# Optimization experiments

Hardware: AMD Instinct MI355X
Metric: run time of the kernel (lower is better)

The kernel has to match this reference:

```python
import jax, jax.numpy as jnp
import numpy as np
from jax import lax

T, H, I, E, K = 1024, 1024, 512, 16, 4


def setup_inputs() -> dict:
    key = jax.random.key(0)
    k1, k2, k3, k4, k5 = jax.random.split(key, 5)
    hidden_states = jax.random.normal(k1, (T, H), dtype=jnp.float32)
    top_k_index = jax.random.randint(k2, (T, K), 0, E)
    top_k_weights = jax.random.uniform(k3, (T, K), dtype=jnp.float32)
    gate_up_proj = jax.random.normal(k4, (E, 2 * I, H), dtype=jnp.float32) * 0.02
    down_proj = jax.random.normal(k5, (E, H, I), dtype=jnp.float32) * 0.02
    return {
        "hidden_states": hidden_states,
        "top_k_index": top_k_index,
        "top_k_weights": top_k_weights,
        "gate_up_proj": gate_up_proj,
        "down_proj": down_proj,
    }


def reference(hidden_states, top_k_index, top_k_weights, gate_up_proj, down_proj):
    num_experts = gate_up_proj.shape[0]
    # combine[t, e] = sum_k top_k_weights[t, k] * [top_k_index[t, k] == e]
    # Expert output is linear in the routing weight, so summing weights over
    # duplicate (token, expert) hits matches the original index_add_ exactly.
    one_hot = jax.nn.one_hot(top_k_index, num_experts, dtype=hidden_states.dtype)  # [T, K, E]
    combine = jnp.einsum("tke,tk->te", one_hot, top_k_weights)  # [T, E]

    def expert_step(acc, xs):
        w_gu, w_d, c = xs  # [2I, H], [H, I], [T]
        gu = hidden_states @ w_gu.T          # [T, 2I]
        gate, up = jnp.split(gu, 2, axis=-1)
        h = jax.nn.silu(gate) * up            # [T, I]
        out = h @ w_d.T                       # [T, H]
        return acc + out * c[:, None], None

    final, _ = lax.scan(
        expert_step,
        jnp.zeros_like(hidden_states),
        (gate_up_proj, down_proj, combine.T),
    )
    return final
```

## Files before the change

### kernel.cpp

```cpp
#include <hip/hip_runtime.h>
#include <hip/hip_bf16.h>
#include <cstdint>
#include <cstddef>

#define T_TOK 1024
#define HDIM  1024
#define IDIM  512
#define NEXP  16
#define TOPK  4
#define CAP   1024

typedef __bf16 bf16;
typedef __attribute__((ext_vector_type(8))) __bf16 bf16x8;
typedef __attribute__((ext_vector_type(4))) __bf16 bf16x4;
typedef __attribute__((ext_vector_type(4))) float f32x4;

__device__ __forceinline__ void lds_load16(void* lds_dst, const void* g_src) {
  __builtin_amdgcn_global_load_lds(
      (__attribute__((address_space(1))) unsigned int*)(void*)(g_src),
      (__attribute__((address_space(3))) unsigned int*)(lds_dst),
      16, 0, 0);
}

__device__ __forceinline__ bf16x4 cvt4(float4 a) {
  bf16x4 o;
  o[0] = (bf16)a.x; o[1] = (bf16)a.y; o[2] = (bf16)a.z; o[3] = (bf16)a.w;
  return o;
}


#define CVT_BLOCKS (T_TOK * HDIM / 4 / 256)

__global__ void prep_kernel(const float* __restrict__ hid_f, bf16* __restrict__ hid_b,
                            const int* __restrict__ idx, const float* __restrict__ w,
                            int* __restrict__ etk, float* __restrict__ ew,
                            int* __restrict__ cntpad, float* __restrict__ out) {
  __shared__ int cnt;
  const int b = blockIdx.x;
  const int tid = threadIdx.x;
  if (b < CVT_BLOCKS) {
    int i = b * 256 + tid;
    float4 v = ((const float4*)hid_f)[i];
    ((bf16x4*)hid_b)[i] = cvt4(v);
    ((float4*)out)[i] = make_float4(0.f, 0.f, 0.f, 0.f);
    if (b == 0)
      ((bf16x4*)(hid_b + (size_t)T_TOK * HDIM))[tid] = cvt4(make_float4(0.f, 0.f, 0.f, 0.f));
    return;
  }
  const int e = b - CVT_BLOCKS;
  if (tid == 0) cnt = 0;
  __syncthreads();
  for (int j = tid; j < T_TOK * TOPK; j += blockDim.x) {
    if (idx[j] == e) {
      int slot = atomicAdd(&cnt, 1);
      if (slot < CAP) { etk[e * CAP + slot] = j; ew[e * CAP + slot] = w[j]; }
    }
  }
  __syncthreads();
  int c = cnt < CAP ? cnt : CAP;
  int p = (c + 127) & ~127;
  for (int j = c + tid; j < p; j += blockDim.x) {
    etk[e * CAP + j] = (T_TOK << 2);
    ew[e * CAP + j] = 0.f;
  }
  if (tid == 0) cntpad[e] = p;
}


__global__ __launch_bounds__(256, 3) void gemm1_kernel(
    const bf16* __restrict__ hid,
    const float* __restrict__ gup,
    const int* __restrict__ etk, const float* __restrict__ ew,
    const int* __restrict__ cntpad,
    bf16* __restrict__ hsc) {
  __shared__ __align__(16) bf16 As[2][128 * 64];
  __shared__ __align__(16) bf16 Bs[2][64 * 64];
  const int e = blockIdx.y, z = blockIdx.z;
  const int ntiles = cntpad[e] >> 7;
  const int n0 = blockIdx.x * 32;
  const int ebase = e * CAP;
  const int tid = threadIdx.x, lane = tid & 63, wid = tid >> 6;
  const int wm = (wid >> 1) * 64, wi = (wid & 1) * 16;
  const int lcol = lane & 15, lquad = lane >> 4;
  const int l7 = lcol & 7;
  const int srow = tid >> 3;
  const int swz = ((tid & 7) ^ (srow & 7)) * 8;
  const int r = tid >> 2;
  const int c0 = (tid & 3) * 4;
  const int grow = (r < 32) ? (n0 + r) : (IDIM + n0 + (r - 32));
  const float* gB = gup + (size_t)e * (2 * IDIM) * HDIM + (size_t)grow * HDIM + c0;
  int wb[4];
#pragma unroll
  for (int j = 0; j < 4; ++j) {
    int c = c0 + 16 * j;
    wb[j] = (((c >> 3) ^ (r & 7)) * 8) + (c & 7);
  }
  const int bst = r * 64;

  for (int mt = z; mt < ntiles; mt += 3) {
    const int mrow = ebase + mt * 128;
    const bf16* gA[4];
#pragma unroll
    for (int q = 0; q < 4; ++q)
      gA[q] = hid + (size_t)(etk[mrow + srow + 32 * q] >> 2) * HDIM + swz;
    f32x4 aG[4], aU[4];
#pragma unroll
    for (int mf = 0; mf < 4; ++mf) {
      aG[mf] = f32x4{0.f, 0.f, 0.f, 0.f};
      aU[mf] = f32x4{0.f, 0.f, 0.f, 0.f};
    }
    {
      float4 bv[4];
#pragma unroll
      for (int j = 0; j < 4; ++j) bv[j] = *(const float4*)(gB + 16 * j);
#pragma unroll
      for (int q = 0; q < 4; ++q)
        lds_load16(&As[0][tid * 8 + q * 2048], gA[q]);
#pragma unroll
      for (int j = 0; j < 4; ++j)
        *(bf16x4*)&Bs[0][bst + wb[j]] = cvt4(bv[j]);
    }
    __syncthreads();
#pragma unroll 2
    for (int k = 0; k < 16; ++k) {
      const int cur = k & 1, nxt = cur ^ 1;
      float4 bn[4];
      if (k < 15) {
#pragma unroll
        for (int q = 0; q < 4; ++q)
          lds_load16(&As[nxt][tid * 8 + q * 2048], gA[q] + (k + 1) * 64);
#pragma unroll
        for (int j = 0; j < 4; ++j)
          bn[j] = *(const float4*)(gB + (k + 1) * 64 + 16 * j);
      }
      __builtin_amdgcn_s_setprio(1);
#pragma unroll
      for (int ks = 0; ks < 2; ++ks) {
        const int lch = ks * 4 + lquad;
        const int sw = (lch ^ l7) * 8;
        bf16x8 bg = *(const bf16x8*)&Bs[cur][(wi + lcol) * 64 + sw];
        bf16x8 bu = *(const bf16x8*)&Bs[cur][(32 + wi + lcol) * 64 + sw];
#pragma unroll
        for (int mf = 0; mf < 4; ++mf) {
          bf16x8 af = *(const bf16x8*)&As[cur][(wm + mf * 16 + lcol) * 64 + sw];
          aG[mf] = __builtin_amdgcn_mfma_f32_16x16x32_bf16(af, bg, aG[mf], 0, 0, 0);
          aU[mf] = __builtin_amdgcn_mfma_f32_16x16x32_bf16(af, bu, aU[mf], 0, 0, 0);
        }
      }
      __builtin_amdgcn_s_setprio(0);
      if (k < 15) {
#pragma unroll
        for (int j = 0; j < 4; ++j)
          *(bf16x4*)&Bs[nxt][bst + wb[j]] = cvt4(bn[j]);
      }
      __syncthreads();
    }
#pragma unroll
    for (int mf = 0; mf < 4; ++mf) {
#pragma unroll
      for (int rr = 0; rr < 4; ++rr) {
        const int erow = mt * 128 + wm + mf * 16 + lquad * 4 + rr;
        const float wgt = ew[ebase + erow];
        float g = aG[mf][rr], u = aU[mf][rr];
        float s = g / (1.f + __expf(-g));
        hsc[(size_t)(ebase + erow) * IDIM + n0 + wi + lcol] = (bf16)(s * u * wgt);
      }
    }
  }
}


__global__ __launch_bounds__(256, 3) void gemm2_kernel(
    const bf16* __restrict__ hsc,
    const float* __restrict__ down,
    const int* __restrict__ etk, const int* __restrict__ cntpad,
    float* __restrict__ out) {
  __shared__ __align__(16) bf16 As[2][128 * 64];
  __shared__ __align__(16) bf16 Bs[2][64 * 64];
  const int e = blockIdx.y, z = blockIdx.z;
  const int ntiles = cntpad[e] >> 7;
  const int n0 = blockIdx.x * 64;
  const int ebase = e * CAP;
  const int tid = threadIdx.x, lane = tid & 63, wid = tid >> 6;
  const int wm = (wid >> 1) * 64, wh = (wid & 1) * 32;
  const int lcol = lane & 15, lquad = lane >> 4;
  const int l7 = lcol & 7;
  const int srow = tid >> 3;
  const int swz = ((tid & 7) ^ (srow & 7)) * 8;
  const int r = tid >> 2;
  const int c0 = (tid & 3) * 4;
  const float* gB = down + (size_t)e * HDIM * IDIM + (size_t)(n0 + r) * IDIM + c0;
  int wb[4];
#pragma unroll
  for (int j = 0; j < 4; ++j) {
    int c = c0 + 16 * j;
    wb[j] = (((c >> 3) ^ (r & 7)) * 8) + (c & 7);
  }
  const int bst = r * 64;

  for (int mt = z; mt < ntiles; mt += 3) {
    const size_t rbase = (size_t)(ebase + mt * 128);
    const bf16* gA[4];
#pragma unroll
    for (int q = 0; q < 4; ++q)
      gA[q] = hsc + (rbase + srow + 32 * q) * IDIM + swz;
    f32x4 acc[4][2];
#pragma unroll
    for (int mf = 0; mf < 4; ++mf) {
      acc[mf][0] = f32x4{0.f, 0.f, 0.f, 0.f};
      acc[mf][1] = f32x4{0.f, 0.f, 0.f, 0.f};
    }
    {
      float4 bv[4];
#pragma unroll
      for (int j = 0; j < 4; ++j) bv[j] = *(const float4*)(gB + 16 * j);
#pragma unroll
      for (int q = 0; q < 4; ++q)
        lds_load16(&As[0][tid * 8 + q * 2048], gA[q]);
#pragma unroll
      for (int j = 0; j < 4; ++j)
        *(bf16x4*)&Bs[0][bst + wb[j]] = cvt4(bv[j]);
    }
    __syncthreads();
#pragma unroll 2
    for (int k = 0; k < 8; ++k) {
      const int cur = k & 1, nxt = cur ^ 1;
      float4 bn[4];
      if (k < 7) {
#pragma unroll
        for (int q = 0; q < 4; ++q)
          lds_load16(&As[nxt][tid * 8 + q * 2048], gA[q] + (k + 1) * 64);
#pragma unroll
        for (int j = 0; j < 4; ++j)
          bn[j] = *(const float4*)(gB + (k + 1) * 64 + 16 * j);
      }
      __builtin_amdgcn_s_setprio(1);
#pragma unroll
      for (int ks = 0; ks < 2; ++ks) {
        const int lch = ks * 4 + lquad;
        const int sw = (lch ^ l7) * 8;
        bf16x8 b0 = *(const bf16x8*)&Bs[cur][(wh + lcol) * 64 + sw];
        bf16x8 b1 = *(const bf16x8*)&Bs[cur][(wh + 16 + lcol) * 64 + sw];
#pragma unroll
        for (int mf = 0; mf < 4; ++mf) {
          bf16x8 af = *(const bf16x8*)&As[cur][(wm + mf * 16 + lcol) * 64 + sw];
          acc[mf][0] = __builtin_amdgcn_mfma_f32_16x16x32_bf16(af, b0, acc[mf][0], 0, 0, 0);
          acc[mf][1] = __builtin_amdgcn_mfma_f32_16x16x32_bf16(af, b1, acc[mf][1], 0, 0, 0);
        }
      }
      __builtin_amdgcn_s_setprio(0);
      if (k < 7) {
#pragma unroll
        for (int j = 0; j < 4; ++j)
          *(bf16x4*)&Bs[nxt][bst + wb[j]] = cvt4(bn[j]);
      }
      __syncthreads();
    }
#pragma unroll
    for (int mf = 0; mf < 4; ++mf) {
#pragma unroll
      for (int rr = 0; rr < 4; ++rr) {
        const int row = mt * 128 + wm + mf * 16 + lquad * 4 + rr;
        const int tk = etk[ebase + row];
        const int tok = tk >> 2;
        if (tok < T_TOK) {
          float* orow = out + (size_t)tok * HDIM + n0 + wh + lcol;
          atomicAdd(orow, acc[mf][0][rr]);
          atomicAdd(orow + 16, acc[mf][1][rr]);
        }
      }
    }
  }
}


extern "C" void kernel_launch(void* const* d_in, const int* in_sizes, int n_in,
                              void* d_out, int out_size, void* d_ws, size_t ws_size,
                              hipStream_t stream) {
  const float* hid_f  = (const float*)d_in[0];
  const int*   idx    = (const int*)d_in[1];
  const float* tw     = (const float*)d_in[2];
  const float* gup_f  = (const float*)d_in[3];
  const float* down_f = (const float*)d_in[4];
  float* out = (float*)d_out;

  uint8_t* ws = (uint8_t*)d_ws;
  size_t off = 0;
  bf16* hid_b = (bf16*)(ws + off);   off += (size_t)(T_TOK + 1) * HDIM * 2;
  int*  etk   = (int*)(ws + off);    off += (size_t)NEXP * CAP * 4;
  float* ewt  = (float*)(ws + off);  off += (size_t)NEXP * CAP * 4;
  int* cntpad = (int*)(ws + off);    off += 256;
  bf16* hsc   = (bf16*)(ws + off);

  prep_kernel<<<dim3(CVT_BLOCKS + NEXP), dim3(256), 0, stream>>>(
      hid_f, hid_b, idx, tw, etk, ewt, cntpad, out);
  gemm1_kernel<<<dim3(IDIM / 32, NEXP, 3), dim3(256), 0, stream>>>(
      hid_b, gup_f, etk, ewt, cntpad, hsc);
  gemm2_kernel<<<dim3(HDIM / 64, NEXP, 3), dim3(256), 0, stream>>>(
      hsc, down_f, etk, cntpad, out);
}
```

Baseline: 176.9 us.

## Flatten expert tiles into grid and stream B operand through registers

Both GEMM kernels now launch one block per (expert, 128-row tile) through a flattened lookup over the padded per-expert counts. This replaces the old grid-stride loop over a fixed z dimension, which left blocks idle for experts with few tiles. The weight operand is no longer staged in LDS: each lane loads its own fp32 fragment from global memory into registers, converts it to bf16 and feeds it straight to the MFMAs. Synchronisation moves to explicit vmcnt waits with a single barrier per k-step. The cost is redundant weight reads across waves, which now lean on the cache. It also risks a write-after-read hazard, because the next A prefetch into LDS can start before slower waves have finished reading that buffer.

```diff
diff --git a/kernel.cpp b/kernel.cpp
--- a/kernel.cpp
+++ b/kernel.cpp
@@ -9,11 +9,17 @@
 #define NEXP  16
 #define TOPK  4
 #define CAP   1024
+#define MAXTILES 48
 
 typedef __bf16 bf16;
 typedef __attribute__((ext_vector_type(8))) __bf16 bf16x8;
 typedef __attribute__((ext_vector_type(4))) __bf16 bf16x4;
 typedef __attribute__((ext_vector_type(4))) float f32x4;
+
+#define WAIT_VM12  asm volatile("s_waitcnt vmcnt(12)" ::: "memory")
+#define WAIT_VM0   asm volatile("s_waitcnt vmcnt(0)" ::: "memory")
+#define BAR() do { asm volatile("" ::: "memory"); __builtin_amdgcn_s_barrier(); \
+                   asm volatile("" ::: "memory"); } while (0)
 
 __device__ __forceinline__ void lds_load16(void* lds_dst, const void* g_src) {
   __builtin_amdgcn_global_load_lds(
@@ -26,6 +32,24 @@
   bf16x4 o;
   o[0] = (bf16)a.x; o[1] = (bf16)a.y; o[2] = (bf16)a.z; o[3] = (bf16)a.w;
   return o;
+}
+
+__device__ __forceinline__ bf16x8 pack8(float4 a, float4 b) {
+  bf16x8 o;
+  o[0] = (bf16)a.x; o[1] = (bf16)a.y; o[2] = (bf16)a.z; o[3] = (bf16)a.w;
+  o[4] = (bf16)b.x; o[5] = (bf16)b.y; o[6] = (bf16)b.z; o[7] = (bf16)b.w;
+  return o;
+}
+
+__device__ __forceinline__ bool tile_lookup(const int* cntpad, int idx,
+                                            int& e_out, int& mt_out) {
+  int rem = idx;
+  for (int e = 0; e < NEXP; ++e) {
+    int nt = cntpad[e] >> 7;
+    if (rem < nt) { e_out = e; mt_out = rem; return true; }
+    rem -= nt;
+  }
+  return false;
 }
 
 
@@ -74,9 +98,8 @@
     const int* __restrict__ cntpad,
     bf16* __restrict__ hsc) {
   __shared__ __align__(16) bf16 As[2][128 * 64];
-  __shared__ __align__(16) bf16 Bs[2][64 * 64];
-  const int e = blockIdx.y, z = blockIdx.z;
-  const int ntiles = cntpad[e] >> 7;
+  int e, mt;
+  if (!tile_lookup(cntpad, blockIdx.y, e, mt)) return;
   const int n0 = blockIdx.x * 32;
   const int ebase = e * CAP;
   const int tid = threadIdx.x, lane = tid & 63, wid = tid >> 6;
@@ -85,86 +108,97 @@
   const int l7 = lcol & 7;
   const int srow = tid >> 3;
   const int swz = ((tid & 7) ^ (srow & 7)) * 8;
-  const int r = tid >> 2;
-  const int c0 = (tid & 3) * 4;
-  const int grow = (r < 32) ? (n0 + r) : (IDIM + n0 + (r - 32));
-  const float* gB = gup + (size_t)e * (2 * IDIM) * HDIM + (size_t)grow * HDIM + c0;
-  int wb[4];
-#pragma unroll
-  for (int j = 0; j < 4; ++j) {
-    int c = c0 + 16 * j;
-    wb[j] = (((c >> 3) ^ (r & 7)) * 8) + (c & 7);
-  }
-  const int bst = r * 64;
-
-  for (int mt = z; mt < ntiles; mt += 3) {
-    const int mrow = ebase + mt * 128;
-    const bf16* gA[4];
+  const int mrow = ebase + mt * 128;
+  const bf16* gA[4];
+#pragma unroll
+  for (int q = 0; q < 4; ++q)
+    gA[q] = hid + (size_t)(etk[mrow + srow + 32 * q] >> 2) * HDIM + swz;
+  const float* gBg = gup + (size_t)e * (2 * IDIM) * HDIM
+                   + (size_t)(n0 + wi + lcol) * HDIM + lquad * 8;
+  const float* gBu = gBg + (size_t)IDIM * HDIM;
+
+  f32x4 aG[4], aU[4];
+#pragma unroll
+  for (int mf = 0; mf < 4; ++mf) {
+    aG[mf] = f32x4{0.f, 0.f, 0.f, 0.f};
+    aU[mf] = f32x4{0.f, 0.f, 0.f, 0.f};
+  }
+  float4 bgv[2][2], buv[2][2];
+#pragma unroll
+  for (int q = 0; q < 4; ++q)
+    lds_load16(&As[0][tid * 8 + q * 2048], gA[q]);
+#pragma unroll
+  for (int ks = 0; ks < 2; ++ks)
+#pragma unroll
+    for (int j = 0; j < 2; ++j) {
+      bgv[ks][j] = *(const float4*)(gBg + ks * 32 + 4 * j);
+      buv[ks][j] = *(const float4*)(gBu + ks * 32 + 4 * j);
+    }
+
+  for (int k = 0; k < 15; ++k) {
+    const int cur = k & 1, nxt = cur ^ 1;
 #pragma unroll
     for (int q = 0; q < 4; ++q)
-      gA[q] = hid + (size_t)(etk[mrow + srow + 32 * q] >> 2) * HDIM + swz;
-    f32x4 aG[4], aU[4];
+      lds_load16(&As[nxt][tid * 8 + q * 2048], gA[q] + (k + 1) * 64);
+    float4 bgn[2][2], bun[2][2];
+#pragma unroll
+    for (int ks = 0; ks < 2; ++ks)
+#pragma unroll
+      for (int j = 0; j < 2; ++j) {
+        bgn[ks][j] = *(const float4*)(gBg + (k + 1) * 64 + ks * 32 + 4 * j);
+        bun[ks][j] = *(const float4*)(gBu + (k + 1) * 64 + ks * 32 + 4 * j);
+      }
+    WAIT_VM12;
+    __builtin_amdgcn_sched_barrier(0);
+    BAR();
+    __builtin_amdgcn_s_setprio(1);
+#pragma unroll
+    for (int ks = 0; ks < 2; ++ks) {
+      const int sw = ((ks * 4 + lquad) ^ l7) * 8;
+      bf16x8 bg = pack8(bgv[ks][0], bgv[ks][1]);
+      bf16x8 bu = pack8(buv[ks][0], buv[ks][1]);
+#pragma unroll
+      for (int mf = 0; mf < 4; ++mf) {
+        bf16x8 af = *(const bf16x8*)&As[cur][(wm + mf * 16 + lcol) * 64 + sw];
+        aG[mf] = __builtin_amdgcn_mfma_f32_16x16x32_bf16(af, bg, aG[mf], 0, 0, 0);
+        aU[mf] = __builtin_amdgcn_mfma_f32_16x16x32_bf16(af, bu, aU[mf], 0, 0, 0);
+      }
+    }
+    __builtin_amdgcn_s_setprio(0);
+#pragma unroll
+    for (int ks = 0; ks < 2; ++ks)
+#pragma unroll
+      for (int j = 0; j < 2; ++j) {
+        bgv[ks][j] = bgn[ks][j];
+        buv[ks][j] = bun[ks][j];
+      }
+  }
+  WAIT_VM0;
+  __builtin_amdgcn_sched_barrier(0);
+  BAR();
+  __builtin_amdgcn_s_setprio(1);
+#pragma unroll
+  for (int ks = 0; ks < 2; ++ks) {
+    const int sw = ((ks * 4 + lquad) ^ l7) * 8;
+    bf16x8 bg = pack8(bgv[ks][0], bgv[ks][1]);
+    bf16x8 bu = pack8(buv[ks][0], buv[ks][1]);
 #pragma unroll
     for (int mf = 0; mf < 4; ++mf) {
-      aG[mf] = f32x4{0.f, 0.f, 0.f, 0.f};
-      aU[mf] = f32x4{0.f, 0.f, 0.f, 0.f};
-    }
-    {
-      float4 bv[4];
-#pragma unroll
-      for (int j = 0; j < 4; ++j) bv[j] = *(const float4*)(gB + 16 * j);
-#pragma unroll
-      for (int q = 0; q < 4; ++q)
-        lds_load16(&As[0][tid * 8 + q * 2048], gA[q]);
-#pragma unroll
-      for (int j = 0; j < 4; ++j)
-        *(bf16x4*)&Bs[0][bst + wb[j]] = cvt4(bv[j]);
-    }
-    __syncthreads();
-#pragma unroll 2
-    for (int k = 0; k < 16; ++k) {
-      const int cur = k & 1, nxt = cur ^ 1;
-      float4 bn[4];
-      if (k < 15) {
-#pragma unroll
-        for (int q = 0; q < 4; ++q)
-          lds_load16(&As[nxt][tid * 8 + q * 2048], gA[q] + (k + 1) * 64);
-#pragma unroll
-        for (int j = 0; j < 4; ++j)
-          bn[j] = *(const float4*)(gB + (k + 1) * 64 + 16 * j);
-      }
-      __builtin_amdgcn_s_setprio(1);
-#pragma unroll
-      for (int ks = 0; ks < 2; ++ks) {
-        const int lch = ks * 4 + lquad;
-        const int sw = (lch ^ l7) * 8;
-        bf16x8 bg = *(const bf16x8*)&Bs[cur][(wi + lcol) * 64 + sw];
-        bf16x8 bu = *(const bf16x8*)&Bs[cur][(32 + wi + lcol) * 64 + sw];
-#pragma unroll
-        for (int mf = 0; mf < 4; ++mf) {
-          bf16x8 af = *(const bf16x8*)&As[cur][(wm + mf * 16 + lcol) * 64 + sw];
-          aG[mf] = __builtin_amdgcn_mfma_f32_16x16x32_bf16(af, bg, aG[mf], 0, 0, 0);
-          aU[mf] = __builtin_amdgcn_mfma_f32_16x16x32_bf16(af, bu, aU[mf], 0, 0, 0);
-        }
-      }
-      __builtin_amdgcn_s_setprio(0);
-      if (k < 15) {
-#pragma unroll
-        for (int j = 0; j < 4; ++j)
-          *(bf16x4*)&Bs[nxt][bst + wb[j]] = cvt4(bn[j]);
-      }
-      __syncthreads();
-    }
-#pragma unroll
-    for (int mf = 0; mf < 4; ++mf) {
-#pragma unroll
-      for (int rr = 0; rr < 4; ++rr) {
-        const int erow = mt * 128 + wm + mf * 16 + lquad * 4 + rr;
-        const float wgt = ew[ebase + erow];
-        float g = aG[mf][rr], u = aU[mf][rr];
-        float s = g / (1.f + __expf(-g));
-        hsc[(size_t)(ebase + erow) * IDIM + n0 + wi + lcol] = (bf16)(s * u * wgt);
-      }
+      bf16x8 af = *(const bf16x8*)&As[1][(wm + mf * 16 + lcol) * 64 + sw];
+      aG[mf] = __builtin_amdgcn_mfma_f32_16x16x32_bf16(af, bg, aG[mf], 0, 0, 0);
+      aU[mf] = __builtin_amdgcn_mfma_f32_16x16x32_bf16(af, bu, aU[mf], 0, 0, 0);
+    }
+  }
+  __builtin_amdgcn_s_setprio(0);
+#pragma unroll
+  for (int mf = 0; mf < 4; ++mf) {
+#pragma unroll
+    for (int rr = 0; rr < 4; ++rr) {
+      const int erow = mt * 128 + wm + mf * 16 + lquad * 4 + rr;
+      const float wgt = ew[ebase + erow];
+      float g = aG[mf][rr], u = aU[mf][rr];
+      float s = g / (1.f + __expf(-g));
+      hsc[(size_t)(ebase + erow) * IDIM + n0 + wi + lcol] = (bf16)(s * u * wgt);
     }
   }
 }
@@ -176,9 +210,8 @@
     const int* __restrict__ etk, const int* __restrict__ cntpad,
     float* __restrict__ out) {
   __shared__ __align__(16) bf16 As[2][128 * 64];
-  __shared__ __align__(16) bf16 Bs[2][64 * 64];
-  const int e = blockIdx.y, z = blockIdx.z;
-  const int ntiles = cntpad[e] >> 7;
+  int e, mt;
+  if (!tile_lookup(cntpad, blockIdx.y, e, mt)) return;
   const int n0 = blockIdx.x * 64;
   const int ebase = e * CAP;
   const int tid = threadIdx.x, lane = tid & 63, wid = tid >> 6;
@@ -187,87 +220,99 @@
   const int l7 = lcol & 7;
   const int srow = tid >> 3;
   const int swz = ((tid & 7) ^ (srow & 7)) * 8;
-  const int r = tid >> 2;
-  const int c0 = (tid & 3) * 4;
-  const float* gB = down + (size_t)e * HDIM * IDIM + (size_t)(n0 + r) * IDIM + c0;
-  int wb[4];
-#pragma unroll
-  for (int j = 0; j < 4; ++j) {
-    int c = c0 + 16 * j;
-    wb[j] = (((c >> 3) ^ (r & 7)) * 8) + (c & 7);
-  }
-  const int bst = r * 64;
-
-  for (int mt = z; mt < ntiles; mt += 3) {
-    const size_t rbase = (size_t)(ebase + mt * 128);
-    const bf16* gA[4];
+  const size_t rbase = (size_t)(ebase + mt * 128);
+  const bf16* gA[4];
+#pragma unroll
+  for (int q = 0; q < 4; ++q)
+    gA[q] = hsc + (rbase + srow + 32 * q) * IDIM + swz;
+  const float* gB0 = down + (size_t)e * HDIM * IDIM
+                   + (size_t)(n0 + wh + lcol) * IDIM + lquad * 8;
+  const float* gB1 = gB0 + (size_t)16 * IDIM;
+
+  f32x4 acc[4][2];
+#pragma unroll
+  for (int mf = 0; mf < 4; ++mf) {
+    acc[mf][0] = f32x4{0.f, 0.f, 0.f, 0.f};
+    acc[mf][1] = f32x4{0.f, 0.f, 0.f, 0.f};
+  }
+  float4 b0v[2][2], b1v[2][2];
+#pragma unroll
+  for (int q = 0; q < 4; ++q)
+    lds_load16(&As[0][tid * 8 + q * 2048], gA[q]);
+#pragma unroll
+  for (int ks = 0; ks < 2; ++ks)
+#pragma unroll
+    for (int j = 0; j < 2; ++j) {
+      b0v[ks][j] = *(const float4*)(gB0 + ks * 32 + 4 * j);
+      b1v[ks][j] = *(const float4*)(gB1 + ks * 32 + 4 * j);
+    }
+
+  for (int k = 0; k < 7; ++k) {
+    const int cur = k & 1, nxt = cur ^ 1;
 #pragma unroll
     for (int q = 0; q < 4; ++q)
-      gA[q] = hsc + (rbase + srow + 32 * q) * IDIM + swz;
-    f32x4 acc[4][2];
+      lds_load16(&As[nxt][tid * 8 + q * 2048], gA[q] + (k + 1) * 64);
+    float4 b0n[2][2], b1n[2][2];
+#pragma unroll
+    for (int ks = 0; ks < 2; ++ks)
+#pragma unroll
+      for (int j = 0; j < 2; ++j) {
+        b0n[ks][j] = *(const float4*)(gB0 + (k + 1) * 64 + ks * 32 + 4 * j);
+        b1n[ks][j] = *(const float4*)(gB1 + (k + 1) * 64 + ks * 32 + 4 * j);
+      }
+    WAIT_VM12;
+    __builtin_amdgcn_sched_barrier(0);
+    BAR();
+    __builtin_amdgcn_s_setprio(1);
+#pragma unroll
+    for (int ks = 0; ks < 2; ++ks) {
+      const int sw = ((ks * 4 + lquad) ^ l7) * 8;
+      bf16x8 b0 = pack8(b0v[ks][0], b0v[ks][1]);
+      bf16x8 b1 = pack8(b1v[ks][0], b1v[ks][1]);
+#pragma unroll
+      for (int mf = 0; mf < 4; ++mf) {
+        bf16x8 af = *(const bf16x8*)&As[cur][(wm + mf * 16 + lcol) * 64 + sw];
+        acc[mf][0] = __builtin_amdgcn_mfma_f32_16x16x32_bf16(af, b0, acc[mf][0], 0, 0, 0);
+        acc[mf][1] = __builtin_amdgcn_mfma_f32_16x16x32_bf16(af, b1, acc[mf][1], 0, 0, 0);
+      }
+    }
+    __builtin_amdgcn_s_setprio(0);
+#pragma unroll
+    for (int ks = 0; ks < 2; ++ks)
+#pragma unroll
+      for (int j = 0; j < 2; ++j) {
+        b0v[ks][j] = b0n[ks][j];
+        b1v[ks][j] = b1n[ks][j];
+      }
+  }
+  WAIT_VM0;
+  __builtin_amdgcn_sched_barrier(0);
+  BAR();
+  __builtin_amdgcn_s_setprio(1);
+#pragma unroll
+  for (int ks = 0; ks < 2; ++ks) {
+    const int sw = ((ks * 4 + lquad) ^ l7) * 8;
+    bf16x8 b0 = pack8(b0v[ks][0], b0v[ks][1]);
+    bf16x8 b1 = pack8(b1v[ks][0], b1v[ks][1]);
 #pragma unroll
     for (int mf = 0; mf < 4; ++mf) {
-      acc[mf][0] = f32x4{0.f, 0.f, 0.f, 0.f};
-      acc[mf][1] = f32x4{0.f, 0.f, 0.f, 0.f};
-    }
-    {
-      float4 bv[4];
-#pragma unroll
-      for (int j = 0; j < 4; ++j) bv[j] = *(const float4*)(gB + 16 * j);
-#pragma unroll
-      for (int q = 0; q < 4; ++q)
-        lds_load16(&As[0][tid * 8 + q * 2048], gA[q]);
-#pragma unroll
-      for (int j = 0; j < 4; ++j)
-        *(bf16x4*)&Bs[0][bst + wb[j]] = cvt4(bv[j]);
-    }
-    __syncthreads();
-#pragma unroll 2
-    for (int k = 0; k < 8; ++k) {
-      const int cur = k & 1, nxt = cur ^ 1;
-      float4 bn[4];
-      if (k < 7) {
-#pragma unroll
-        for (int q = 0; q < 4; ++q)
-          lds_load16(&As[nxt][tid * 8 + q * 2048], gA[q] + (k + 1) * 64);
-#pragma unroll
-        for (int j = 0; j < 4; ++j)
-          bn[j] = *(const float4*)(gB + (k + 1) * 64 + 16 * j);
-      }
-      __builtin_amdgcn_s_setprio(1);
-#pragma unroll
-      for (int ks = 0; ks < 2; ++ks) {
-        const int lch = ks * 4 + lquad;
-        const int sw = (lch ^ l7) * 8;
-        bf16x8 b0 = *(const bf16x8*)&Bs[cur][(wh + lcol) * 64 + sw];
-        bf16x8 b1 = *(const bf16x8*)&Bs[cur][(wh + 16 + lcol) * 64 + sw];
-#pragma unroll
-        for (int mf = 0; mf < 4; ++mf) {
-          bf16x8 af = *(const bf16x8*)&As[cur][(wm + mf * 16 + lcol) * 64 + sw];
-          acc[mf][0] = __builtin_amdgcn_mfma_f32_16x16x32_bf16(af, b0, acc[mf][0], 0, 0, 0);
-          acc[mf][1] = __builtin_amdgcn_mfma_f32_16x16x32_bf16(af, b1, acc[mf][1], 0, 0, 0);
-        }
-      }
-      __builtin_amdgcn_s_setprio(0);
-      if (k < 7) {
-#pragma unroll
-        for (int j = 0; j < 4; ++j)
-          *(bf16x4*)&Bs[nxt][bst + wb[j]] = cvt4(bn[j]);
-      }
-      __syncthreads();
-    }
-#pragma unroll
-    for (int mf = 0; mf < 4; ++mf) {
-#pragma unroll
-      for (int rr = 0; rr < 4; ++rr) {
-        const int row = mt * 128 + wm + mf * 16 + lquad * 4 + rr;
-        const int tk = etk[ebase + row];
-        const int tok = tk >> 2;
-        if (tok < T_TOK) {
-          float* orow = out + (size_t)tok * HDIM + n0 + wh + lcol;
-          atomicAdd(orow, acc[mf][0][rr]);
-          atomicAdd(orow + 16, acc[mf][1][rr]);
-        }
+      bf16x8 af = *(const bf16x8*)&As[1][(wm + mf * 16 + lcol) * 64 + sw];
+      acc[mf][0] = __builtin_amdgcn_mfma_f32_16x16x32_bf16(af, b0, acc[mf][0], 0, 0, 0);
+      acc[mf][1] = __builtin_amdgcn_mfma_f32_16x16x32_bf16(af, b1, acc[mf][1], 0, 0, 0);
+    }
+  }
+  __builtin_amdgcn_s_setprio(0);
+#pragma unroll
+  for (int mf = 0; mf < 4; ++mf) {
+#pragma unroll
+    for (int rr = 0; rr < 4; ++rr) {
+      const int row = mt * 128 + wm + mf * 16 + lquad * 4 + rr;
+      const int tk = etk[ebase + row];
+      const int tok = tk >> 2;
+      if (tok < T_TOK) {
+        float* orow = out + (size_t)tok * HDIM + n0 + wh + lcol;
+        atomicAdd(orow, acc[mf][0][rr]);
+        atomicAdd(orow + 16, acc[mf][1][rr]);
       }
     }
   }
@@ -294,8 +339,8 @@
 
   prep_kernel<<<dim3(CVT_BLOCKS + NEXP), dim3(256), 0, stream>>>(
       hid_f, hid_b, idx, tw, etk, ewt, cntpad, out);
-  gemm1_kernel<<<dim3(IDIM / 32, NEXP, 3), dim3(256), 0, stream>>>(
+  gemm1_kernel<<<dim3(IDIM / 32, MAXTILES), dim3(256), 0, stream>>>(
       hid_b, gup_f, etk, ewt, cntpad, hsc);
-  gemm2_kernel<<<dim3(HDIM / 64, NEXP, 3), dim3(256), 0, stream>>>(
+  gemm2_kernel<<<dim3(HDIM / 64, MAXTILES), dim3(256), 0, stream>>>(
       hsc, down_f, etk, cntpad, out);
 }
```

Measured after the change: 214.1 us. +21.0%, slower.
